# Performance work log

Measured on AMD Instinct MI355X. Metric: run time of the kernel, lower is better.

Reference implementation:

```python
import math
import jax, jax.numpy as jnp
import numpy as np

V = 256; PS = 4; D = 256; MAXR = 4; MINR = 2; WIN = 4; KRET = 8; LAMP = 0.2

def _ln(x, g, b):
    m = x.mean(-1, keepdims=True)
    v = ((x - m) ** 2).mean(-1, keepdims=True)
    return (x - m) / jnp.sqrt(v + 1e-5) * g + b

def _gelu(x):
    return jax.nn.gelu(x, approximate=False)  # torch nn.GELU default = exact erf

def setup_inputs():
    key = jax.random.key(0)
    ks = iter(jax.random.split(key, 64))
    def w(shape, s=0.02):
        return jax.random.normal(next(ks), shape, jnp.float32) * s
    B, T = 32, 2048
    x = jax.random.randint(next(ks), (B, T), 0, V)
    z = lambda *s: jnp.zeros(s, jnp.float32)
    o = lambda *s: jnp.ones(s, jnp.float32)
    return dict(
        x=x,
        emb=w((V, D)), pos=w((PS, D)),
        gru_wih=w((3 * D, D)), gru_whh=w((3 * D, D)), gru_bih=z(3 * D), gru_bhh=z(3 * D),
        pp_ln_g=o(D), pp_ln_b=z(D),
        sum_w=w((D, D)), sum_b=z(D),
        msg_w1=w((2 * D, D)), msg_b1=z(D), msg_w2=w((D, D)), msg_b2=z(D),
        upd_w1=w((2 * D, D)), upd_b1=z(D), upd_w2=w((D, D)), upd_b2=z(D),
        halt_w=w((D, 1)), halt_b=z(1),
        mp_ln_g=o(D), mp_ln_b=z(D),
        q_w=w((D, D)), q_b=z(D), k_w=w((D, D)), k_b=z(D),
        v_w=w((D, D)), v_b=z(D), o_w=w((D, D)), o_b=z(D),
        br_w=w((D, D)), br_b=z(D),
        f_ln_g=o(D), f_ln_b=z(D),
        head_w=w((D, V)),
    )

def _forward(x, emb, pos, gru_wih, gru_whh, gru_bih, gru_bhh, pp_ln_g, pp_ln_b,
             sum_w, sum_b, msg_w1, msg_b1, msg_w2, msg_b2, upd_w1, upd_b1,
             upd_w2, upd_b2, halt_w, halt_b, mp_ln_g, mp_ln_b,
             q_w, q_b, k_w, k_b, v_w, v_b, o_w, o_b, br_w, br_b,
             f_ln_g, f_ln_b, head_w):
    B, T = x.shape
    N = T // PS  # T chosen divisible by patch_size, so F.pad is a no-op
    patches = x.reshape(B * N, PS)
    # --- GRU patch processor (all patches processed identically -> batch them) ---
    hin = emb[patches] + pos[None, :, :]            # [BN, PS, D]
    xg = hin @ gru_wih.T + gru_bih                  # [BN, PS, 3D]
    def gru_step(hprev, xp):
        gh = hprev @ gru_whh.T + gru_bhh
        ir, iz, inn = jnp.split(xp, 3, axis=-1)
        hr, hz, hn = jnp.split(gh, 3, axis=-1)
        r = jax.nn.sigmoid(ir + hr)
        zg = jax.nn.sigmoid(iz + hz)
        n = jnp.tanh(inn + r * hn)
        h = (1 - zg) * n + zg * hprev
        return h, h
    h0 = jnp.zeros((B * N, D), xg.dtype)
    _, seq = jax.lax.scan(gru_step, h0, jnp.swapaxes(xg, 0, 1))
    local = _ln(jnp.swapaxes(seq, 0, 1), pp_ln_g, pp_ln_b).reshape(B, N, PS, D)
    summaries = local.mean(2) @ sum_w + sum_b       # [B, N, D]
    # --- local message passing with ACT halting (vectorized sliding window) ---
    idx = jnp.arange(N)[:, None] + jnp.arange(-WIN, 1)[None, :]
    valid = idx >= 0
    idxc = jnp.clip(idx, 0, N - 1)
    counts = valid.sum(1).astype(jnp.float32)                     # [N]
    h = summaries
    remaining = jnp.ones((B, N, 1), jnp.float32)
    output = jnp.zeros_like(h)
    kl = jnp.float32(0.0)
    for step in range(MAXR):
        nb = h[:, idxc]
        sr = jnp.broadcast_to(h[:, :, None, :], nb.shape)
        m = _gelu(jnp.concatenate([sr, nb], -1) @ msg_w1 + msg_b1) @ msg_w2 + msg_b2
        msgs = (m * valid[None, :, :, None]).sum(2) / counts[None, :, None]
        upd = _gelu(jnp.concatenate([h, msgs], -1) @ upd_w1 + upd_b1) @ upd_w2 + upd_b2
        h = _ln(h + upd, mp_ln_g, mp_ln_b)
        if step < MINR:
            hp = jnp.zeros((B, 1, 1), jnp.float32)
        elif step == MAXR - 1:
            hp = jnp.ones((B, 1, 1), jnp.float32)
        else:
            hp = jax.nn.sigmoid(h.mean(1, keepdims=True) @ halt_w + halt_b)  # [B,1,1]
        output = output + remaining * hp * h
        remaining = remaining * (1 - hp)
        p = LAMP * (1 - LAMP) ** step
        kl = kl + p * (math.log(p) - jnp.log(hp.mean() + 1e-8))
    kl = kl / MAXR
    # --- sparse top-k causal retrieval over patch summaries ---
    q = output @ q_w + q_b
    k = output @ k_w + k_b
    v = output @ v_w + v_b
    scores = jnp.einsum('bnd,bmd->bnm', q, k) / math.sqrt(D)
    causal = jnp.tril(jnp.ones((N, N), bool))
    scores = jnp.where(causal[None], scores, -jnp.inf)
    tv, ti = jax.lax.top_k(scores, KRET)
    bI = jnp.arange(B)[:, None, None]
    nI = jnp.arange(N)[None, :, None]
    sparse = jnp.full_like(scores, -jnp.inf).at[bI, nI, ti].set(tv)
    attn = jax.nn.softmax(sparse, axis=-1)
    retrieved = jnp.einsum('bnm,bmd->bnd', attn, v) @ o_w + o_b
    combined = output + retrieved
    broad = combined @ br_w + br_b                                # [B, N, D]
    final = (local + broad[:, :, None, :]).reshape(B, N * PS, D)
    logits = _ln(final, f_ln_g, f_ln_b) @ head_w                  # [B, T, V]
    return logits, kl

def reference(x, emb, pos, gru_wih, gru_whh, gru_bih, gru_bhh, pp_ln_g, pp_ln_b,
              sum_w, sum_b, msg_w1, msg_b1, msg_w2, msg_b2, upd_w1, upd_b1,
              upd_w2, upd_b2, halt_w, halt_b, mp_ln_g, mp_ln_b,
              q_w, q_b, k_w, k_b, v_w, v_b, o_w, o_b, br_w, br_b,
              f_ln_g, f_ln_b, head_w):
    return _forward(x, emb, pos, gru_wih, gru_whh, gru_bih, gru_bhh, pp_ln_g, pp_ln_b,
                    sum_w, sum_b, msg_w1, msg_b1, msg_w2, msg_b2, upd_w1, upd_b1,
                    upd_w2, upd_b2, halt_w, halt_b, mp_ln_g, mp_ln_b,
                    q_w, q_b, k_w, k_b, v_w, v_b, o_w, o_b, br_w, br_b,
                    f_ln_g, f_ln_b, head_w)
```

## Files before the change

### kernel.cpp

```cpp
#include <hip/hip_runtime.h>
#include <cmath>


constexpr int N_   = 512;
constexpr int B_   = 32;
constexpr int BN_  = B_ * N_;
constexpr int M1_  = BN_ * 4;

typedef short bf16x8 __attribute__((ext_vector_type(8)));
typedef float f32x4  __attribute__((ext_vector_type(4)));

__device__ __forceinline__ float gelu_f(float x) {
  return 0.5f * x * (1.0f + erff(x * 0.70710678118654752440f));
}
__device__ __forceinline__ float sigm_f(float x) {
  return 1.0f / (1.0f + expf(-x));
}
__device__ __forceinline__ unsigned short f2bf(float f) {
  union { float f; unsigned int u; } c; c.f = f;
  unsigned int u = c.u;
  u += 0x7FFFu + ((u >> 16) & 1u);
  return (unsigned short)(u >> 16);
}
__device__ __forceinline__ float bf2f(unsigned short u) {
  union { unsigned int u; float f; } c; c.u = ((unsigned int)u) << 16;
  return c.f;
}
__device__ __forceinline__ int phys(int g, int r) {
  return ((g << 6) | (r ^ g)) << 3;
}
__device__ __forceinline__ int phys128(int g, int r) {
  return ((g << 7) | (r ^ g)) << 3;
}
__device__ __forceinline__ int phys16(int g, int r) {
  return ((g << 4) | (r ^ g)) << 3;
}

template<int AMODE, int EPI, int COUT>
__global__ __launch_bounds__(256)
void gemm_big(const void* __restrict__ A, const unsigned short* __restrict__ Bt,
              const float* __restrict__ bias, void* __restrict__ C,
              int M, int Nn, int K, int bstride, int ldC)
{
  __shared__ short As[4 * 128 * 8];
  __shared__ short Bs[4 * 128 * 8];
  const int t  = threadIdx.x;
  const int m0 = blockIdx.y * 128, n0 = blockIdx.x * 128;
  const int lane = t & 63, w = t >> 6;
  const int wr = w >> 1, wc = w & 1;
  const int fr = lane & 15, fg = lane >> 4;

  f32x4 acc[4][4] = {};

  for (int k0 = 0; k0 < K; k0 += 32) {
    #pragma unroll
    for (int c = 0; c < 2; ++c) {
      int idx = t + c * 256;
      int row = idx >> 2, g = idx & 3;
      int kk = k0 + g * 8;
      bf16x8 av;
      if constexpr (AMODE == 1) {
        av = *(const bf16x8*)&((const unsigned short*)A)[(size_t)(m0 + row) * K + kk];
      } else {
        const float4* p = (const float4*)&((const float*)A)[(size_t)(m0 + row) * K + kk];
        float4 a = p[0], b = p[1];
        av[0]=(short)f2bf(a.x); av[1]=(short)f2bf(a.y); av[2]=(short)f2bf(a.z); av[3]=(short)f2bf(a.w);
        av[4]=(short)f2bf(b.x); av[5]=(short)f2bf(b.y); av[6]=(short)f2bf(b.z); av[7]=(short)f2bf(b.w);
      }
      *(bf16x8*)&As[phys128(g, row)] = av;
      *(bf16x8*)&Bs[phys128(g, row)] =
          *(const bf16x8*)&Bt[(size_t)(n0 + row) * bstride + kk];
    }
    __syncthreads();

    bf16x8 a[4], b[4];
    #pragma unroll
    for (int i = 0; i < 4; ++i)
      a[i] = *(const bf16x8*)&As[phys128(fg, wr * 64 + i * 16 + fr)];
    #pragma unroll
    for (int j = 0; j < 4; ++j)
      b[j] = *(const bf16x8*)&Bs[phys128(fg, wc * 64 + j * 16 + fr)];
    #pragma unroll
    for (int i = 0; i < 4; ++i)
      #pragma unroll
      for (int j = 0; j < 4; ++j)
        acc[i][j] = __builtin_amdgcn_mfma_f32_16x16x32_bf16(a[i], b[j], acc[i][j], 0, 0, 0);
    __syncthreads();
  }

  #pragma unroll
  for (int i = 0; i < 4; ++i)
    #pragma unroll
    for (int j = 0; j < 4; ++j) {
      int col = n0 + wc * 64 + j * 16 + fr;
      float bcol = bias ? bias[col] : 0.0f;
      #pragma unroll
      for (int r = 0; r < 4; ++r) {
        int row = m0 + wr * 64 + i * 16 + fg * 4 + r;
        float vv = acc[i][j][r] + bcol;
        if constexpr (EPI == 1) vv = gelu_f(vv);
        if constexpr (COUT == 0)
          ((float*)C)[(size_t)row * ldC + col] = vv;
        else
          ((unsigned short*)C)[(size_t)row * ldC + col] = f2bf(vv);
      }
    }
}

template<int MODE, int BSRC, int EPI, int COUT>
__global__ __launch_bounds__(256)
void gemm_mfma(const float* __restrict__ A, const void* __restrict__ Bsrc,
               const float* __restrict__ bias, void* __restrict__ C,
               int M, int Nn, int K, int bstride, int ldC,
               const float* __restrict__ P2,
               const float* __restrict__ emb, const float* __restrict__ pos)
{
  __shared__ short As[4 * 64 * 8];
  __shared__ short Bs[4 * 64 * 8];
  const int tid  = threadIdx.x;
  const int m0   = blockIdx.y * 64, n0 = blockIdx.x * 64;
  const int srow = tid >> 2, sg = tid & 3;
  const int lane = tid & 63, w = tid >> 6;
  const int wr   = w >> 1,  wc = w & 1;
  const int fr   = lane & 15, fg = lane >> 4;

  f32x4 acc[2][2] = {};

  for (int k0 = 0; k0 < K; k0 += 32) {
    {
      int m = m0 + srow, k = k0 + sg * 8;
      bf16x8 tv;
      if constexpr (MODE == 10) {
        if (k < 256)
          tv = *(const bf16x8*)&((const unsigned short*)A)[(size_t)m * 256 + k];
        else
          tv = *(const bf16x8*)&((const unsigned short*)P2)[(size_t)m * 256 + (k - 256)];
      } else if constexpr (MODE == 11) {
        if (k < 256) {
          const float4* p = (const float4*)(A + (size_t)m * 256 + k);
          float4 a = p[0], b = p[1];
          tv[0]=(short)f2bf(a.x); tv[1]=(short)f2bf(a.y); tv[2]=(short)f2bf(a.z); tv[3]=(short)f2bf(a.w);
          tv[4]=(short)f2bf(b.x); tv[5]=(short)f2bf(b.y); tv[6]=(short)f2bf(b.z); tv[7]=(short)f2bf(b.w);
        } else {
          tv = *(const bf16x8*)&((const unsigned short*)P2)[(size_t)m * 256 + (k - 256)];
        }
      } else {
        float v[8];
        if constexpr (MODE == 6) {
          const float* src = nullptr;
          if (m < 256) src = emb + (size_t)m * 256 + k;
          else if (m < 260) src = pos + (size_t)(m - 256) * 256 + k;
          if (src) {
            const float4* p = (const float4*)src;
            float4 a = p[0], b = p[1];
            v[0]=a.x; v[1]=a.y; v[2]=a.z; v[3]=a.w; v[4]=b.x; v[5]=b.y; v[6]=b.z; v[7]=b.w;
          } else {
            #pragma unroll
            for (int j = 0; j < 8; ++j) v[j] = 0.f;
          }
        } else if constexpr (MODE == 8) {
          #pragma unroll
          for (int j = 0; j < 8; ++j) v[j] = P2[(size_t)(k + j) * 256 + m];
        } else {
          const unsigned short* Ab = (const unsigned short*)A;
          const unsigned short* base = Ab + (size_t)m * 1024 + k;
          bf16x8 r0 = *(const bf16x8*)(base);
          bf16x8 r1 = *(const bf16x8*)(base + 256);
          bf16x8 r2 = *(const bf16x8*)(base + 512);
          bf16x8 r3 = *(const bf16x8*)(base + 768);
          #pragma unroll
          for (int j = 0; j < 8; ++j)
            v[j] = 0.25f * (bf2f((unsigned short)r0[j]) + bf2f((unsigned short)r1[j]) +
                            bf2f((unsigned short)r2[j]) + bf2f((unsigned short)r3[j]));
        }
        #pragma unroll
        for (int j = 0; j < 8; ++j) tv[j] = (short)f2bf(v[j]);
      }
      *(bf16x8*)&As[phys(sg, srow)] = tv;
    }
    if constexpr (BSRC == 0) {
      const unsigned short* Bt = (const unsigned short*)Bsrc;
      *(bf16x8*)&Bs[phys(sg, srow)] =
          *(const bf16x8*)&Bt[(size_t)(n0 + srow) * bstride + k0 + sg * 8];
    } else {
      const float* Bf = (const float*)Bsrc;
      const float4* p = (const float4*)(Bf + (size_t)(n0 + srow) * bstride + k0 + sg * 8);
      float4 a = p[0], b = p[1];
      bf16x8 tv;
      tv[0]=(short)f2bf(a.x); tv[1]=(short)f2bf(a.y); tv[2]=(short)f2bf(a.z); tv[3]=(short)f2bf(a.w);
      tv[4]=(short)f2bf(b.x); tv[5]=(short)f2bf(b.y); tv[6]=(short)f2bf(b.z); tv[7]=(short)f2bf(b.w);
      *(bf16x8*)&Bs[phys(sg, srow)] = tv;
    }
    __syncthreads();

    bf16x8 a0 = *(const bf16x8*)&As[phys(fg, wr * 32 + fr)];
    bf16x8 a1 = *(const bf16x8*)&As[phys(fg, wr * 32 + 16 + fr)];
    bf16x8 b0 = *(const bf16x8*)&Bs[phys(fg, wc * 32 + fr)];
    bf16x8 b1 = *(const bf16x8*)&Bs[phys(fg, wc * 32 + 16 + fr)];
    acc[0][0] = __builtin_amdgcn_mfma_f32_16x16x32_bf16(a0, b0, acc[0][0], 0, 0, 0);
    acc[0][1] = __builtin_amdgcn_mfma_f32_16x16x32_bf16(a0, b1, acc[0][1], 0, 0, 0);
    acc[1][0] = __builtin_amdgcn_mfma_f32_16x16x32_bf16(a1, b0, acc[1][0], 0, 0, 0);
    acc[1][1] = __builtin_amdgcn_mfma_f32_16x16x32_bf16(a1, b1, acc[1][1], 0, 0, 0);
    __syncthreads();
  }

  #pragma unroll
  for (int i = 0; i < 2; ++i) {
    #pragma unroll
    for (int j = 0; j < 2; ++j) {
      int row0 = m0 + wr * 32 + i * 16 + fg * 4;
      int col  = n0 + wc * 32 + j * 16 + fr;
      float bcol = bias ? bias[col] : 0.0f;
      #pragma unroll
      for (int r = 0; r < 4; ++r) {
        float vv = acc[i][j][r] + bcol;
        if constexpr (EPI == 1) vv = gelu_f(vv);
        int row = row0 + r;
        if constexpr (COUT == 0)
          ((float*)C)[(size_t)row * ldC + col] = vv;
        else
          ((unsigned short*)C)[(size_t)row * ldC + col] = f2bf(vv);
      }
    }
  }
}

template<int OUTM>
__global__ __launch_bounds__(256)
void gemm_ln(const unsigned short* __restrict__ U, const unsigned short* __restrict__ u2T,
             const float* __restrict__ bias, unsigned short* __restrict__ h,
             const float* __restrict__ g, const float* __restrict__ bb,
             const float* __restrict__ hp, float* __restrict__ outp)
{
  __shared__ short As[4 * 16 * 8];
  __shared__ short Bs[4 * 256 * 8];
  __shared__ float psum[4][16], pssq[4][16];
  const int m0 = blockIdx.x * 16;
  const int t  = threadIdx.x;
  const int lane = t & 63, w = t >> 6;
  const int fr = lane & 15, fg = lane >> 4;

  f32x4 acc[4] = {};
  for (int k0 = 0; k0 < 256; k0 += 32) {
    if (t < 64) {
      int row = t >> 2, gq = t & 3;
      *(bf16x8*)&As[phys16(gq, row)] =
          *(const bf16x8*)&U[(size_t)(m0 + row) * 256 + k0 + gq * 8];
    }
    const unsigned short* brow = u2T + (size_t)t * 256 + k0;
    #pragma unroll
    for (int gq = 0; gq < 4; ++gq)
      *(bf16x8*)&Bs[((gq << 8) | (t ^ gq)) << 3] = *(const bf16x8*)(brow + gq * 8);
    __syncthreads();
    bf16x8 a = *(const bf16x8*)&As[phys16(fg, fr)];
    #pragma unroll
    for (int j = 0; j < 4; ++j) {
      int n = 64 * w + 16 * j + fr;
      bf16x8 b = *(const bf16x8*)&Bs[((fg << 8) | (n ^ fg)) << 3];
      acc[j] = __builtin_amdgcn_mfma_f32_16x16x32_bf16(a, b, acc[j], 0, 0, 0);
    }
    __syncthreads();
  }

  float bcol[4], gv[4], bv[4];
  #pragma unroll
  for (int j = 0; j < 4; ++j) {
    int col = 64 * w + 16 * j + fr;
    bcol[j] = bias[col]; gv[j] = g[col]; bv[j] = bb[col];
  }
  float vsum[4] = {}, vssq[4] = {};
  #pragma unroll
  for (int j = 0; j < 4; ++j) {
    int col = 64 * w + 16 * j + fr;
    #pragma unroll
    for (int r = 0; r < 4; ++r) {
      int row = m0 + 4 * fg + r;
      float v = acc[j][r] + bcol[j] + bf2f(h[(size_t)row * 256 + col]);
      acc[j][r] = v;
      vsum[r] += v;
      vssq[r] += v * v;
    }
  }
  #pragma unroll
  for (int off = 1; off < 16; off <<= 1) {
    #pragma unroll
    for (int r = 0; r < 4; ++r) {
      vsum[r] += __shfl_xor(vsum[r], off, 64);
      vssq[r] += __shfl_xor(vssq[r], off, 64);
    }
  }
  if (fr == 0) {
    #pragma unroll
    for (int r = 0; r < 4; ++r) {
      psum[w][4 * fg + r] = vsum[r];
      pssq[w][4 * fg + r] = vssq[r];
    }
  }
  __syncthreads();

  float rem = 0.f;
  if constexpr (OUTM == 3) rem = 1.0f - hp[m0 >> 9];
  #pragma unroll
  for (int r = 0; r < 4; ++r) {
    int rr = 4 * fg + r;
    float s  = psum[0][rr] + psum[1][rr] + psum[2][rr] + psum[3][rr];
    float q2 = pssq[0][rr] + pssq[1][rr] + pssq[2][rr] + pssq[3][rr];
    float mean = s * (1.0f / 256.0f);
    float var  = q2 * (1.0f / 256.0f) - mean * mean;
    float inv  = rsqrtf(var + 1e-5f);
    int row = m0 + rr;
    #pragma unroll
    for (int j = 0; j < 4; ++j) {
      int col = 64 * w + 16 * j + fr;
      float y = (acc[j][r] - mean) * inv * gv[j] + bv[j];
      h[(size_t)row * 256 + col] = f2bf(y);
      if constexpr (OUTM == 3) outp[(size_t)row * 256 + col] += rem * y;
    }
  }
}

__global__ __launch_bounds__(256)
void scores_tri(const unsigned short* __restrict__ qkv, float* __restrict__ sc)
{
  int flat = blockIdx.x;
  int xcd = flat & 7, s = flat >> 3;
  int bhi = s / 36, tile = s - bhi * 36;
  int b = bhi * 8 + xcd;
  int ti = 0;
  while ((ti + 1) * (ti + 2) / 2 <= tile) ++ti;
  int tj = tile - ti * (ti + 1) / 2;
  const int m0 = ti * 64, n0 = tj * 64;
  const unsigned short* Aq = qkv + (size_t)b * N_ * 768;
  const unsigned short* Bk = Aq + 256;

  __shared__ short As[4 * 64 * 8];
  __shared__ short Bs[4 * 64 * 8];
  const int tid  = threadIdx.x;
  const int srow = tid >> 2, sg = tid & 3;
  const int lane = tid & 63, w = tid >> 6;
  const int wr   = w >> 1,  wc = w & 1;
  const int fr   = lane & 15, fg = lane >> 4;

  f32x4 acc[2][2] = {};
  for (int k0 = 0; k0 < 256; k0 += 32) {
    *(bf16x8*)&As[phys(sg, srow)] =
        *(const bf16x8*)&Aq[(size_t)(m0 + srow) * 768 + k0 + sg * 8];
    *(bf16x8*)&Bs[phys(sg, srow)] =
        *(const bf16x8*)&Bk[(size_t)(n0 + srow) * 768 + k0 + sg * 8];
    __syncthreads();
    bf16x8 a0 = *(const bf16x8*)&As[phys(fg, wr * 32 + fr)];
    bf16x8 a1 = *(const bf16x8*)&As[phys(fg, wr * 32 + 16 + fr)];
    bf16x8 b0 = *(const bf16x8*)&Bs[phys(fg, wc * 32 + fr)];
    bf16x8 b1 = *(const bf16x8*)&Bs[phys(fg, wc * 32 + 16 + fr)];
    acc[0][0] = __builtin_amdgcn_mfma_f32_16x16x32_bf16(a0, b0, acc[0][0], 0, 0, 0);
    acc[0][1] = __builtin_amdgcn_mfma_f32_16x16x32_bf16(a0, b1, acc[0][1], 0, 0, 0);
    acc[1][0] = __builtin_amdgcn_mfma_f32_16x16x32_bf16(a1, b0, acc[1][0], 0, 0, 0);
    acc[1][1] = __builtin_amdgcn_mfma_f32_16x16x32_bf16(a1, b1, acc[1][1], 0, 0, 0);
    __syncthreads();
  }
  float* scb = sc + (size_t)b * N_ * N_;
  #pragma unroll
  for (int i = 0; i < 2; ++i) {
    #pragma unroll
    for (int j = 0; j < 2; ++j) {
      int row0 = m0 + wr * 32 + i * 16 + fg * 4;
      int col  = n0 + wc * 32 + j * 16 + fr;
      #pragma unroll
      for (int r = 0; r < 4; ++r) {
        int row = row0 + r;
        float vv = acc[i][j][r] * 0.0625f;
        if (col > row) vv = -__builtin_inff();
        scb[(size_t)row * N_ + col] = vv;
      }
    }
  }
}

struct PrepJobs {
  const float* src[12];
  unsigned short* dst[12];
  int rows[12];
  int dstride[12];
  int strt[12];
};
__global__ __launch_bounds__(256)
void prep_w_k(PrepJobs pj)
{
  int jid = blockIdx.y;
  const float* src = pj.src[jid];
  unsigned short* dst = pj.dst[jid];
  int ds = pj.dstride[jid];
  int total = pj.rows[jid] << 8;
  if (pj.strt[jid]) {
    for (int i = blockIdx.x * 256 + threadIdx.x; i < total; i += gridDim.x * 256) {
      int k = i & 255, n = i >> 8;
      dst[(size_t)n * ds + k] = f2bf(src[i]);
    }
  } else {
    for (int i = blockIdx.x * 256 + threadIdx.x; i < total; i += gridDim.x * 256) {
      int k = i & 255, n = i >> 8;
      dst[(size_t)n * ds + k] = f2bf(src[(size_t)k * 256 + n]);
    }
  }
}

__global__ __launch_bounds__(256)
void biasprep_k(const float* __restrict__ upd_b1, const float* __restrict__ msg_b2,
                const float* __restrict__ upd_w1, const float* __restrict__ msg_b1,
                const float* __restrict__ o_b, const float* __restrict__ br_w,
                const float* __restrict__ br_b, const float* __restrict__ q_b,
                const float* __restrict__ k_b, const float* __restrict__ v_b,
                float* __restrict__ biasU, float* __restrict__ biasHsn,
                float* __restrict__ biasB2, float* __restrict__ bQKV)
{
  int c = threadIdx.x;
  float s = upd_b1[c];
  for (int k = 0; k < 256; ++k)
    s += msg_b2[k] * upd_w1[(size_t)(256 + k) * 256 + c];
  biasU[c] = s;
  biasHsn[c] = msg_b1[c];
  biasHsn[256 + c] = 0.f;
  float s2 = br_b[c];
  for (int k = 0; k < 256; ++k)
    s2 += o_b[k] * br_w[(size_t)k * 256 + c];
  biasB2[c] = s2;
  bQKV[c] = q_b[c]; bQKV[256 + c] = k_b[c]; bQKV[512 + c] = v_b[c];
}

template<int FIRST>
__global__ __launch_bounds__(256)
void gru_pw_k(const unsigned short* __restrict__ gh, const float* __restrict__ bhh,
              const float* __restrict__ embW, const int* __restrict__ x,
              const float* __restrict__ bih,
              unsigned short* __restrict__ h, unsigned short* __restrict__ local, int t)
{
  int i   = blockIdx.x * 256 + threadIdx.x;
  int row = i >> 8, d = i & 255;
  int tok = x[row * 4 + t];
  const float* er = embW + (size_t)tok * 768;
  const float* pr = embW + (size_t)(256 + t) * 768;
  float ir  = er[d]       + pr[d]       + bih[d];
  float iz  = er[256 + d] + pr[256 + d] + bih[256 + d];
  float inn = er[512 + d] + pr[512 + d] + bih[512 + d];
  float hr, hz, hn;
  if constexpr (FIRST) {
    hr = bhh[d]; hz = bhh[256 + d]; hn = bhh[512 + d];
  } else {
    const unsigned short* gr = gh + (size_t)row * 768;
    hr = bf2f(gr[d]); hz = bf2f(gr[256 + d]); hn = bf2f(gr[512 + d]);
  }
  float r  = sigm_f(ir + hr);
  float zg = sigm_f(iz + hz);
  float nn = tanhf(inn + r * hn);
  float hnew;
  if constexpr (FIRST) hnew = (1.0f - zg) * nn;
  else                 hnew = (1.0f - zg) * nn + zg * bf2f(h[i]);
  h[i] = f2bf(hnew);
  local[((size_t)row * 4 + t) * 256 + d] = f2bf(hnew);
}

__global__ __launch_bounds__(256)
void smsg_k(const unsigned short* __restrict__ hsn, unsigned short* __restrict__ S)
{
  int i = blockIdx.x * 256 + threadIdx.x;
  int m = i >> 6, d4 = (i & 63) << 2;
  int n = m & (N_ - 1);
  ushort4 hsu = *(const ushort4*)&hsn[(size_t)m * 512 + d4];
  float hs0 = bf2f(hsu.x), hs1 = bf2f(hsu.y), hs2 = bf2f(hsu.z), hs3 = bf2f(hsu.w);
  float a0 = 0.f, a1 = 0.f, a2 = 0.f, a3 = 0.f;
  #pragma unroll
  for (int kk = 0; kk < 5; ++kk) {
    int idx = n + kk - 4;
    if (idx >= 0) {
      ushort4 hv = *(const ushort4*)&hsn[(size_t)(m + kk - 4) * 512 + 256 + d4];
      a0 += gelu_f(hs0 + bf2f(hv.x));
      a1 += gelu_f(hs1 + bf2f(hv.y));
      a2 += gelu_f(hs2 + bf2f(hv.z));
      a3 += gelu_f(hs3 + bf2f(hv.w));
    }
  }
  float sc1 = 1.0f / (float)((n < 4 ? n : 4) + 1);
  ushort4 o = {f2bf(a0 * sc1), f2bf(a1 * sc1), f2bf(a2 * sc1), f2bf(a3 * sc1)};
  *(ushort4*)&S[(size_t)m * 256 + d4] = o;
}

__global__ __launch_bounds__(256)
void ln_bf16_k(unsigned short* __restrict__ X, const float* __restrict__ g,
               const float* __restrict__ bb)
{
  int wave = threadIdx.x >> 6, lane = threadIdx.x & 63;
  int row  = blockIdx.x * 4 + wave;
  unsigned short* xr = X + (size_t)row * 256;
  ushort4 u = *(const ushort4*)&xr[lane * 4];
  float x[4] = {bf2f(u.x), bf2f(u.y), bf2f(u.z), bf2f(u.w)};
  float s = x[0] + x[1] + x[2] + x[3];
  #pragma unroll
  for (int off = 1; off < 64; off <<= 1) s += __shfl_xor(s, off, 64);
  float mean = s * (1.0f / 256.0f);
  float ss = 0.f;
  #pragma unroll
  for (int j = 0; j < 4; ++j) { float d = x[j] - mean; ss += d * d; }
  #pragma unroll
  for (int off = 1; off < 64; off <<= 1) ss += __shfl_xor(ss, off, 64);
  float inv = rsqrtf(ss * (1.0f / 256.0f) + 1e-5f);
  ushort4 o;
  o.x = f2bf((x[0] - mean) * inv * g[lane*4+0] + bb[lane*4+0]);
  o.y = f2bf((x[1] - mean) * inv * g[lane*4+1] + bb[lane*4+1]);
  o.z = f2bf((x[2] - mean) * inv * g[lane*4+2] + bb[lane*4+2]);
  o.w = f2bf((x[3] - mean) * inv * g[lane*4+3] + bb[lane*4+3]);
  *(ushort4*)&xr[lane * 4] = o;
}

__global__ __launch_bounds__(256)
void ln_cvt_k(const unsigned short* __restrict__ X, const unsigned short* __restrict__ Add,
              const float* __restrict__ g, const float* __restrict__ bb,
              unsigned short* __restrict__ Out)
{
  int wave = threadIdx.x >> 6, lane = threadIdx.x & 63;
  int row  = blockIdx.x * 4 + wave;
  ushort4 u = *(const ushort4*)&X[(size_t)row * 256 + lane * 4];
  ushort4 a = *(const ushort4*)&Add[(size_t)(row >> 2) * 256 + lane * 4];
  float x[4] = {bf2f(u.x) + bf2f(a.x), bf2f(u.y) + bf2f(a.y),
                bf2f(u.z) + bf2f(a.z), bf2f(u.w) + bf2f(a.w)};
  float s = x[0] + x[1] + x[2] + x[3];
  #pragma unroll
  for (int off = 1; off < 64; off <<= 1) s += __shfl_xor(s, off, 64);
  float mean = s * (1.0f / 256.0f);
  float ss = 0.f;
  #pragma unroll
  for (int j = 0; j < 4; ++j) { float d = x[j] - mean; ss += d * d; }
  #pragma unroll
  for (int off = 1; off < 64; off <<= 1) ss += __shfl_xor(ss, off, 64);
  float inv = rsqrtf(ss * (1.0f / 256.0f) + 1e-5f);
  ushort4 o;
  o.x = f2bf((x[0] - mean) * inv * g[lane*4+0] + bb[lane*4+0]);
  o.y = f2bf((x[1] - mean) * inv * g[lane*4+1] + bb[lane*4+1]);
  o.z = f2bf((x[2] - mean) * inv * g[lane*4+2] + bb[lane*4+2]);
  o.w = f2bf((x[3] - mean) * inv * g[lane*4+3] + bb[lane*4+3]);
  *(ushort4*)&Out[(size_t)row * 256 + lane * 4] = o;
}

__global__ __launch_bounds__(256)
void halt1_k(const unsigned short* __restrict__ h, const float* __restrict__ hw,
             float* __restrict__ part)
{
  int b = blockIdx.x, s = blockIdx.y, tid = threadIdx.x;
  const unsigned short* p = h + ((size_t)b * N_ + s * 32) * 256;
  float acc = 0.f;
  for (int i = tid * 4; i < 32 * 256; i += 1024) {
    ushort4 u = *(const ushort4*)&p[i];
    const float4 w4 = *(const float4*)&hw[i & 255];
    acc += bf2f(u.x) * w4.x + bf2f(u.y) * w4.y + bf2f(u.z) * w4.z + bf2f(u.w) * w4.w;
  }
  __shared__ float red[256];
  red[tid] = acc; __syncthreads();
  for (int off = 128; off > 0; off >>= 1) {
    if (tid < off) red[tid] += red[tid + off];
    __syncthreads();
  }
  if (tid == 0) part[b * 16 + s] = red[0];
}
__global__ __launch_bounds__(64)
void halt2_k(const float* __restrict__ part, const float* __restrict__ hb,
             float* __restrict__ hp)
{
  int b = threadIdx.x;
  if (b < 32) {
    float s = 0.f;
    for (int i = 0; i < 16; ++i) s += part[b * 16 + i];
    hp[b] = sigm_f(s * (1.0f / (float)N_) + hb[0]);
  }
}
__global__ __launch_bounds__(256)
void out2_k(const unsigned short* __restrict__ h, const float* __restrict__ hp,
            float* __restrict__ outp)
{
  int i = blockIdx.x * 256 + threadIdx.x;
  outp[i] = hp[i >> 17] * bf2f(h[i]);
}

__global__ __launch_bounds__(256)
void topk_k(const float* __restrict__ sc, const unsigned short* __restrict__ qkv,
            unsigned short* __restrict__ rpre)
{
  const float NEG = -__builtin_inff();
  int wave = threadIdx.x >> 6, lane = threadIdx.x & 63;
  int rowg = blockIdx.x * 4 + wave;
  int b = rowg >> 9, n = rowg & (N_ - 1);
  const float* srow = sc + (size_t)rowg * N_;
  float v[8];
  #pragma unroll
  for (int j = 0; j < 8; ++j) {
    int col = lane + j * 64;
    v[j] = (col <= n) ? srow[col] : NEG;
  }
  float tv[8]; int ti[8];
  #pragma unroll
  for (int it = 0; it < 8; ++it) {
    float bv = v[0]; int bi = lane;
    #pragma unroll
    for (int j = 1; j < 8; ++j)
      if (v[j] > bv) { bv = v[j]; bi = lane + j * 64; }
    #pragma unroll
    for (int off = 1; off < 64; off <<= 1) {
      float ov = __shfl_xor(bv, off, 64);
      int   oi = __shfl_xor(bi, off, 64);
      if (ov > bv || (ov == bv && oi < bi)) { bv = ov; bi = oi; }
    }
    tv[it] = bv; ti[it] = bi;
    if ((bi & 63) == lane) v[bi >> 6] = NEG;
  }
  float mx = tv[0];
  float wsum = 0.f, wj[8];
  #pragma unroll
  for (int j = 0; j < 8; ++j) { wj[j] = expf(tv[j] - mx); wsum += wj[j]; }
  float inv = 1.0f / wsum;
  const unsigned short* vb = qkv + 512;
  int d0 = lane * 4;
  float a0 = 0.f, a1 = 0.f, a2 = 0.f, a3 = 0.f;
  #pragma unroll
  for (int j = 0; j < 8; ++j) {
    float wgt = wj[j] * inv;
    ushort4 vv = *(const ushort4*)&vb[((size_t)(b * N_ + ti[j])) * 768 + d0];
    a0 += wgt * bf2f(vv.x); a1 += wgt * bf2f(vv.y);
    a2 += wgt * bf2f(vv.z); a3 += wgt * bf2f(vv.w);
  }
  ushort4 o = {f2bf(a0), f2bf(a1), f2bf(a2), f2bf(a3)};
  *(ushort4*)&rpre[(size_t)rowg * 256 + d0] = o;
}

__global__ void kl_k(const float* __restrict__ hp, float* __restrict__ out)
{
  if (threadIdx.x == 0 && blockIdx.x == 0) {
    float hm = 0.f;
    for (int b = 0; b < 32; ++b) hm += hp[b];
    hm *= (1.0f / 32.0f);
    const float l1e8 = logf(1e-8f);
    float kl = 0.f;
    kl += 0.2f    * (logf(0.2f)    - l1e8);
    kl += 0.16f   * (logf(0.16f)   - l1e8);
    kl += 0.128f  * (logf(0.128f)  - logf(hm + 1e-8f));
    kl += 0.1024f * (logf(0.1024f) - logf(1.0f + 1e-8f));
    out[0] = kl * 0.25f;
  }
}

extern "C" void kernel_launch(void* const* d_in, const int* in_sizes, int n_in,
                              void* d_out, int out_size, void* d_ws, size_t ws_size,
                              hipStream_t stream)
{
  const int*   x       = (const int*)  d_in[0];
  const float* emb     = (const float*)d_in[1];
  const float* pos     = (const float*)d_in[2];
  const float* gru_wih = (const float*)d_in[3];
  const float* gru_whh = (const float*)d_in[4];
  const float* gru_bih = (const float*)d_in[5];
  const float* gru_bhh = (const float*)d_in[6];
  const float* pp_ln_g = (const float*)d_in[7];
  const float* pp_ln_b = (const float*)d_in[8];
  const float* sum_w   = (const float*)d_in[9];
  const float* sum_b   = (const float*)d_in[10];
  const float* msg_w1  = (const float*)d_in[11];
  const float* msg_b1  = (const float*)d_in[12];
  const float* msg_w2  = (const float*)d_in[13];
  const float* msg_b2  = (const float*)d_in[14];
  const float* upd_w1  = (const float*)d_in[15];
  const float* upd_b1  = (const float*)d_in[16];
  const float* upd_w2  = (const float*)d_in[17];
  const float* upd_b2  = (const float*)d_in[18];
  const float* halt_w  = (const float*)d_in[19];
  const float* halt_b  = (const float*)d_in[20];
  const float* mp_ln_g = (const float*)d_in[21];
  const float* mp_ln_b = (const float*)d_in[22];
  const float* q_w     = (const float*)d_in[23];
  const float* q_b     = (const float*)d_in[24];
  const float* k_w     = (const float*)d_in[25];
  const float* k_b     = (const float*)d_in[26];
  const float* v_w     = (const float*)d_in[27];
  const float* v_b     = (const float*)d_in[28];
  const float* o_w     = (const float*)d_in[29];
  const float* o_b     = (const float*)d_in[30];
  const float* br_w    = (const float*)d_in[31];
  const float* br_b    = (const float*)d_in[32];
  const float* f_ln_g  = (const float*)d_in[33];
  const float* f_ln_b  = (const float*)d_in[34];
  const float* head_w  = (const float*)d_in[35];

  constexpr size_t SZ_Q = (size_t)BN_ * 256;
  float* ws     = (float*)d_ws;
  float* R_h    = ws;
  float* R_outp = R_h    + SZ_Q;
  float* R_b1   = R_outp + SZ_Q;
  float* R_b2   = R_b1   + SZ_Q;
  float* R_b3   = R_b2   + SZ_Q;
  float* R_rp   = R_b3   + SZ_Q;
  unsigned short* R_loc = (unsigned short*)(R_rp + SZ_Q);
  unsigned short* wb = R_loc + 4 * SZ_Q;
  unsigned short* sumT  = wb;
  unsigned short* W1cT  = sumT  + 65536;
  unsigned short* u1cT  = W1cT  + 131072;
  unsigned short* u2T   = u1cT  + 131072;
  unsigned short* qkvT  = u2T   + 65536;
  unsigned short* brWT  = qkvT  + 196608;
  unsigned short* headT = brWT  + 131072;
  unsigned short* whhT  = headT + 65536;
  float* R_embW = (float*)(whhT + 196608);
  float* R_bU   = R_embW + 320 * 768;
  float* R_bH   = R_bU + 256;
  float* R_bB2  = R_bH + 512;
  float* R_bQKV = R_bB2 + 256;
  float* R_part = R_bQKV + 768;
  float* R_hp   = R_part + 512;

  unsigned short* R_hb = ((unsigned short*)R_b3) + SZ_Q;

  float* logits = (float*)d_out;
  dim3 blk(256);

  PrepJobs pj;
  const float* srcs[11] = {sum_w, msg_w1, msg_w1 + 65536, upd_w1, upd_w2,
                           q_w, k_w, v_w, br_w, head_w, gru_whh};
  unsigned short* dsts[11] = {sumT, W1cT, W1cT + 65536, u1cT, u2T,
                              qkvT, qkvT + 65536, qkvT + 131072, brWT, headT, whhT};
  int rows[11] = {256,256,256,256,256,256,256,256,256,256,768};
  int dstd[11] = {256,256,256,512,256,256,256,256,512,256,256};
  int strt[11] = {0,0,0,0,0,0,0,0,0,0,1};
  for (int i = 0; i < 11; ++i) {
    pj.src[i]=srcs[i]; pj.dst[i]=dsts[i]; pj.rows[i]=rows[i];
    pj.dstride[i]=dstd[i]; pj.strt[i]=strt[i];
  }
  prep_w_k<<<dim3(64, 11), blk, 0, stream>>>(pj);
  biasprep_k<<<dim3(1), blk, 0, stream>>>(upd_b1, msg_b2, upd_w1, msg_b1,
                                          o_b, br_w, br_b, q_b, k_b, v_b,
                                          R_bU, R_bH, R_bB2, R_bQKV);
  gemm_mfma<8, 1, 0, 1><<<dim3(4, 4), blk, 0, stream>>>(
      nullptr, msg_w2, nullptr, u1cT + 256, 256, 256, 256, 256, 512,
      upd_w1 + 65536, nullptr, nullptr);
  gemm_mfma<8, 1, 0, 1><<<dim3(4, 4), blk, 0, stream>>>(
      nullptr, o_w, nullptr, brWT + 256, 256, 256, 256, 256, 512,
      br_w, nullptr, nullptr);
  gemm_mfma<6, 1, 0, 0><<<dim3(12, 5), blk, 0, stream>>>(
      nullptr, gru_wih, nullptr, R_embW, 320, 768, 256, 256, 768,
      nullptr, emb, pos);

  unsigned short* ghB = (unsigned short*)R_b1;
  gru_pw_k<1><<<dim3(BN_), blk, 0, stream>>>(
      nullptr, gru_bhh, R_embW, x, gru_bih, R_hb, R_loc, 0);
  for (int t = 1; t < 4; ++t) {
    gemm_big<1, 0, 1><<<dim3(6, 128), blk, 0, stream>>>(
        R_hb, whhT, gru_bhh, ghB, BN_, 768, 256, 256, 768);
    gru_pw_k<0><<<dim3(BN_), blk, 0, stream>>>(
        ghB, gru_bhh, R_embW, x, gru_bih, R_hb, R_loc, t);
  }
  ln_bf16_k<<<dim3(M1_ / 4), blk, 0, stream>>>(R_loc, pp_ln_g, pp_ln_b);

  gemm_mfma<9, 0, 0, 1><<<dim3(4, 256), blk, 0, stream>>>(
      (const float*)R_loc, sumT, sum_b, R_hb, BN_, 256, 256, 256, 256,
      nullptr, nullptr, nullptr);

  unsigned short* hsnB = (unsigned short*)R_b1;
  unsigned short* UB   = (unsigned short*)R_b2;
  unsigned short* Sb   = (unsigned short*)R_b3;
  for (int step = 0; step < 4; ++step) {
    gemm_big<1, 0, 1><<<dim3(4, 128), blk, 0, stream>>>(
        R_hb, W1cT, R_bH, hsnB, BN_, 512, 256, 256, 512);
    smsg_k<<<dim3(BN_ / 4), blk, 0, stream>>>(hsnB, Sb);
    gemm_mfma<10, 0, 1, 1><<<dim3(4, 256), blk, 0, stream>>>(
        (const float*)R_hb, u1cT, R_bU, UB, BN_, 256, 512, 512, 256,
        (const float*)Sb, nullptr, nullptr);
    if (step == 3) {
      gemm_ln<3><<<dim3(BN_ / 16), blk, 0, stream>>>(
          UB, u2T, upd_b2, R_hb, mp_ln_g, mp_ln_b, R_hp, R_outp);
    } else {
      gemm_ln<0><<<dim3(BN_ / 16), blk, 0, stream>>>(
          UB, u2T, upd_b2, R_hb, mp_ln_g, mp_ln_b, nullptr, nullptr);
      if (step == 2) {
        halt1_k<<<dim3(32, 16), blk, 0, stream>>>(R_hb, halt_w, R_part);
        halt2_k<<<dim3(1), dim3(64), 0, stream>>>(R_part, halt_b, R_hp);
        out2_k<<<dim3(BN_), blk, 0, stream>>>(R_hb, R_hp, R_outp);
      }
    }
  }

  unsigned short* qkv  = (unsigned short*)R_b3;
  unsigned short* rpre = ((unsigned short*)R_rp) + SZ_Q;
  float* sc = R_b1;
  gemm_big<0, 0, 1><<<dim3(6, 128), blk, 0, stream>>>(
      R_outp, qkvT, R_bQKV, qkv, BN_, 768, 256, 256, 768);
  scores_tri<<<dim3(1152), blk, 0, stream>>>(qkv, sc);
  topk_k<<<dim3(BN_ / 4), blk, 0, stream>>>(sc, qkv, rpre);

  unsigned short* broadB = (unsigned short*)R_h;
  gemm_mfma<11, 0, 0, 1><<<dim3(4, 256), blk, 0, stream>>>(
      R_outp, brWT, R_bB2, broadB, BN_, 256, 512, 512, 256,
      (const float*)rpre, nullptr, nullptr);

  unsigned short* Abuf = (unsigned short*)R_b1;
  ln_cvt_k<<<dim3(M1_ / 4), blk, 0, stream>>>(R_loc, broadB, f_ln_g, f_ln_b, Abuf);
  gemm_big<1, 0, 0><<<dim3(2, 512), blk, 0, stream>>>(
      Abuf, headT, nullptr, logits, M1_, 256, 256, 256, 256);

  kl_k<<<dim3(1), dim3(64), 0, stream>>>(R_hp, logits + (size_t)M1_ * 256);
}
```

Baseline: 611.8 us.

## Fuse final LayerNorm into head GEMM, store scores in bf16, vectorize pointwise kernels

Adds a head_ln_k kernel that computes the final LayerNorm row statistics in-block and normalizes A tiles while loading them, which removes the separate ln_cvt_k pass and its intermediate buffer. Attention scores are now written and read as bf16 rather than fp32, halving that traffic. gru_pw_k and out2_k are vectorized to process four elements per thread. In exchange, LN inputs are recomputed once per column block, the one-pass variance formula is used, and bf16 scores may change top-k tie ordering.

```diff
diff --git a/kernel.cpp b/kernel.cpp
--- a/kernel.cpp
+++ b/kernel.cpp
@@ -103,6 +103,106 @@
           ((float*)C)[(size_t)row * ldC + col] = vv;
         else
           ((unsigned short*)C)[(size_t)row * ldC + col] = f2bf(vv);
+      }
+    }
+}
+
+__global__ __launch_bounds__(256)
+void head_ln_k(const unsigned short* __restrict__ loc,
+               const unsigned short* __restrict__ broad,
+               const float* __restrict__ g, const float* __restrict__ bb,
+               const unsigned short* __restrict__ headT,
+               float* __restrict__ out)
+{
+  __shared__ short As[4 * 128 * 8];
+  __shared__ short Bs[4 * 128 * 8];
+  __shared__ float sMean[128], sInv[128];
+  const int t  = threadIdx.x;
+  const int m0 = blockIdx.y * 128, n0 = blockIdx.x * 128;
+  const int lane = t & 63, w = t >> 6;
+  const int wr = w >> 1, wc = w & 1;
+  const int fr = lane & 15, fg = lane >> 4;
+
+  {
+    int r = t >> 1, half = t & 1;
+    int row = m0 + r;
+    const unsigned short* lp = loc   + (size_t)row * 256 + half * 128;
+    const unsigned short* bp = broad + (size_t)(row >> 2) * 256 + half * 128;
+    float s = 0.f, ss = 0.f;
+    #pragma unroll
+    for (int c = 0; c < 16; ++c) {
+      bf16x8 u = *(const bf16x8*)(lp + c * 8);
+      bf16x8 a = *(const bf16x8*)(bp + c * 8);
+      #pragma unroll
+      for (int e = 0; e < 8; ++e) {
+        float xv = bf2f((unsigned short)u[e]) + bf2f((unsigned short)a[e]);
+        s += xv; ss += xv * xv;
+      }
+    }
+    s  += __shfl_xor(s, 1, 64);
+    ss += __shfl_xor(ss, 1, 64);
+    if (half == 0) {
+      float mean = s * (1.0f / 256.0f);
+      float var  = ss * (1.0f / 256.0f) - mean * mean;
+      sMean[r] = mean;
+      sInv[r]  = rsqrtf(var + 1e-5f);
+    }
+  }
+  __syncthreads();
+
+  f32x4 acc[4][4] = {};
+  for (int k0 = 0; k0 < 256; k0 += 32) {
+    #pragma unroll
+    for (int c = 0; c < 2; ++c) {
+      int idx = t + c * 256;
+      int row = idx >> 2, gq = idx & 3;
+      int kk = k0 + gq * 8;
+      int grow = m0 + row;
+      bf16x8 u = *(const bf16x8*)&loc[(size_t)grow * 256 + kk];
+      bf16x8 a = *(const bf16x8*)&broad[(size_t)(grow >> 2) * 256 + kk];
+      float mean = sMean[row], inv = sInv[row];
+      const float4 g0 = *(const float4*)(g + kk);
+      const float4 g1 = *(const float4*)(g + kk + 4);
+      const float4 v0 = *(const float4*)(bb + kk);
+      const float4 v1 = *(const float4*)(bb + kk + 4);
+      float gv[8] = {g0.x,g0.y,g0.z,g0.w,g1.x,g1.y,g1.z,g1.w};
+      float bv[8] = {v0.x,v0.y,v0.z,v0.w,v1.x,v1.y,v1.z,v1.w};
+      bf16x8 av;
+      #pragma unroll
+      for (int e = 0; e < 8; ++e) {
+        float xv = bf2f((unsigned short)u[e]) + bf2f((unsigned short)a[e]);
+        av[e] = (short)f2bf((xv - mean) * inv * gv[e] + bv[e]);
+      }
+      *(bf16x8*)&As[phys128(gq, row)] = av;
+      *(bf16x8*)&Bs[phys128(gq, row)] =
+          *(const bf16x8*)&headT[(size_t)(n0 + row) * 256 + kk];
+    }
+    __syncthreads();
+
+    bf16x8 a[4], b[4];
+    #pragma unroll
+    for (int i = 0; i < 4; ++i)
+      a[i] = *(const bf16x8*)&As[phys128(fg, wr * 64 + i * 16 + fr)];
+    #pragma unroll
+    for (int j = 0; j < 4; ++j)
+      b[j] = *(const bf16x8*)&Bs[phys128(fg, wc * 64 + j * 16 + fr)];
+    #pragma unroll
+    for (int i = 0; i < 4; ++i)
+      #pragma unroll
+      for (int j = 0; j < 4; ++j)
+        acc[i][j] = __builtin_amdgcn_mfma_f32_16x16x32_bf16(a[i], b[j], acc[i][j], 0, 0, 0);
+    __syncthreads();
+  }
+
+  #pragma unroll
+  for (int i = 0; i < 4; ++i)
+    #pragma unroll
+    for (int j = 0; j < 4; ++j) {
+      int col = n0 + wc * 64 + j * 16 + fr;
+      #pragma unroll
+      for (int r = 0; r < 4; ++r) {
+        int row = m0 + wr * 64 + i * 16 + fg * 4 + r;
+        out[(size_t)row * 256 + col] = acc[i][j][r];
       }
     }
 }
@@ -320,7 +420,7 @@
 }
 
 __global__ __launch_bounds__(256)
-void scores_tri(const unsigned short* __restrict__ qkv, float* __restrict__ sc)
+void scores_tri(const unsigned short* __restrict__ qkv, unsigned short* __restrict__ sc)
 {
   int flat = blockIdx.x;
   int xcd = flat & 7, s = flat >> 3;
@@ -358,7 +458,7 @@
     acc[1][1] = __builtin_amdgcn_mfma_f32_16x16x32_bf16(a1, b1, acc[1][1], 0, 0, 0);
     __syncthreads();
   }
-  float* scb = sc + (size_t)b * N_ * N_;
+  unsigned short* scb = sc + (size_t)b * N_ * N_;
   #pragma unroll
   for (int i = 0; i < 2; ++i) {
     #pragma unroll
@@ -370,7 +470,7 @@
         int row = row0 + r;
         float vv = acc[i][j][r] * 0.0625f;
         if (col > row) vv = -__builtin_inff();
-        scb[(size_t)row * N_ + col] = vv;
+        scb[(size_t)row * N_ + col] = f2bf(vv);
       }
     }
   }
@@ -435,28 +535,55 @@
               unsigned short* __restrict__ h, unsigned short* __restrict__ local, int t)
 {
   int i   = blockIdx.x * 256 + threadIdx.x;
-  int row = i >> 8, d = i & 255;
+  int row = i >> 6, d0 = (i & 63) << 2;
   int tok = x[row * 4 + t];
   const float* er = embW + (size_t)tok * 768;
   const float* pr = embW + (size_t)(256 + t) * 768;
-  float ir  = er[d]       + pr[d]       + bih[d];
-  float iz  = er[256 + d] + pr[256 + d] + bih[256 + d];
-  float inn = er[512 + d] + pr[512 + d] + bih[512 + d];
-  float hr, hz, hn;
+  float4 e0 = *(const float4*)(er + d0);
+  float4 e1 = *(const float4*)(er + 256 + d0);
+  float4 e2 = *(const float4*)(er + 512 + d0);
+  float4 p0 = *(const float4*)(pr + d0);
+  float4 p1 = *(const float4*)(pr + 256 + d0);
+  float4 p2 = *(const float4*)(pr + 512 + d0);
+  float4 q0 = *(const float4*)(bih + d0);
+  float4 q1 = *(const float4*)(bih + 256 + d0);
+  float4 q2 = *(const float4*)(bih + 512 + d0);
+  float ir[4]  = {e0.x+p0.x+q0.x, e0.y+p0.y+q0.y, e0.z+p0.z+q0.z, e0.w+p0.w+q0.w};
+  float iz[4]  = {e1.x+p1.x+q1.x, e1.y+p1.y+q1.y, e1.z+p1.z+q1.z, e1.w+p1.w+q1.w};
+  float inn[4] = {e2.x+p2.x+q2.x, e2.y+p2.y+q2.y, e2.z+p2.z+q2.z, e2.w+p2.w+q2.w};
+  float hr[4], hz[4], hn[4];
   if constexpr (FIRST) {
-    hr = bhh[d]; hz = bhh[256 + d]; hn = bhh[512 + d];
+    float4 b0 = *(const float4*)(bhh + d0);
+    float4 b1 = *(const float4*)(bhh + 256 + d0);
+    float4 b2 = *(const float4*)(bhh + 512 + d0);
+    hr[0]=b0.x; hr[1]=b0.y; hr[2]=b0.z; hr[3]=b0.w;
+    hz[0]=b1.x; hz[1]=b1.y; hz[2]=b1.z; hz[3]=b1.w;
+    hn[0]=b2.x; hn[1]=b2.y; hn[2]=b2.z; hn[3]=b2.w;
   } else {
     const unsigned short* gr = gh + (size_t)row * 768;
-    hr = bf2f(gr[d]); hz = bf2f(gr[256 + d]); hn = bf2f(gr[512 + d]);
-  }
-  float r  = sigm_f(ir + hr);
-  float zg = sigm_f(iz + hz);
-  float nn = tanhf(inn + r * hn);
-  float hnew;
-  if constexpr (FIRST) hnew = (1.0f - zg) * nn;
-  else                 hnew = (1.0f - zg) * nn + zg * bf2f(h[i]);
-  h[i] = f2bf(hnew);
-  local[((size_t)row * 4 + t) * 256 + d] = f2bf(hnew);
+    ushort4 u0 = *(const ushort4*)(gr + d0);
+    ushort4 u1 = *(const ushort4*)(gr + 256 + d0);
+    ushort4 u2 = *(const ushort4*)(gr + 512 + d0);
+    hr[0]=bf2f(u0.x); hr[1]=bf2f(u0.y); hr[2]=bf2f(u0.z); hr[3]=bf2f(u0.w);
+    hz[0]=bf2f(u1.x); hz[1]=bf2f(u1.y); hz[2]=bf2f(u1.z); hz[3]=bf2f(u1.w);
+    hn[0]=bf2f(u2.x); hn[1]=bf2f(u2.y); hn[2]=bf2f(u2.z); hn[3]=bf2f(u2.w);
+  }
+  ushort4 hprev = {0, 0, 0, 0};
+  if constexpr (!FIRST) hprev = *(const ushort4*)&h[(size_t)row * 256 + d0];
+  float hp4[4] = {bf2f(hprev.x), bf2f(hprev.y), bf2f(hprev.z), bf2f(hprev.w)};
+  ushort4 oh;
+  #pragma unroll
+  for (int e = 0; e < 4; ++e) {
+    float r  = sigm_f(ir[e] + hr[e]);
+    float zg = sigm_f(iz[e] + hz[e]);
+    float nn = tanhf(inn[e] + r * hn[e]);
+    float hnew;
+    if constexpr (FIRST) hnew = (1.0f - zg) * nn;
+    else                 hnew = (1.0f - zg) * nn + zg * hp4[e];
+    ((unsigned short*)&oh)[e] = f2bf(hnew);
+  }
+  *(ushort4*)&h[(size_t)row * 256 + d0] = oh;
+  *(ushort4*)&local[((size_t)row * 4 + t) * 256 + d0] = oh;
 }
 
 __global__ __launch_bounds__(256)
@@ -512,35 +639,6 @@
 }
 
 __global__ __launch_bounds__(256)
-void ln_cvt_k(const unsigned short* __restrict__ X, const unsigned short* __restrict__ Add,
-              const float* __restrict__ g, const float* __restrict__ bb,
-              unsigned short* __restrict__ Out)
-{
-  int wave = threadIdx.x >> 6, lane = threadIdx.x & 63;
-  int row  = blockIdx.x * 4 + wave;
-  ushort4 u = *(const ushort4*)&X[(size_t)row * 256 + lane * 4];
-  ushort4 a = *(const ushort4*)&Add[(size_t)(row >> 2) * 256 + lane * 4];
-  float x[4] = {bf2f(u.x) + bf2f(a.x), bf2f(u.y) + bf2f(a.y),
-                bf2f(u.z) + bf2f(a.z), bf2f(u.w) + bf2f(a.w)};
-  float s = x[0] + x[1] + x[2] + x[3];
-  #pragma unroll
-  for (int off = 1; off < 64; off <<= 1) s += __shfl_xor(s, off, 64);
-  float mean = s * (1.0f / 256.0f);
-  float ss = 0.f;
-  #pragma unroll
-  for (int j = 0; j < 4; ++j) { float d = x[j] - mean; ss += d * d; }
-  #pragma unroll
-  for (int off = 1; off < 64; off <<= 1) ss += __shfl_xor(ss, off, 64);
-  float inv = rsqrtf(ss * (1.0f / 256.0f) + 1e-5f);
-  ushort4 o;
-  o.x = f2bf((x[0] - mean) * inv * g[lane*4+0] + bb[lane*4+0]);
-  o.y = f2bf((x[1] - mean) * inv * g[lane*4+1] + bb[lane*4+1]);
-  o.z = f2bf((x[2] - mean) * inv * g[lane*4+2] + bb[lane*4+2]);
-  o.w = f2bf((x[3] - mean) * inv * g[lane*4+3] + bb[lane*4+3]);
-  *(ushort4*)&Out[(size_t)row * 256 + lane * 4] = o;
-}
-
-__global__ __launch_bounds__(256)
 void halt1_k(const unsigned short* __restrict__ h, const float* __restrict__ hw,
              float* __restrict__ part)
 {
@@ -576,23 +674,26 @@
             float* __restrict__ outp)
 {
   int i = blockIdx.x * 256 + threadIdx.x;
-  outp[i] = hp[i >> 17] * bf2f(h[i]);
-}
-
-__global__ __launch_bounds__(256)
-void topk_k(const float* __restrict__ sc, const unsigned short* __restrict__ qkv,
+  float hpv = hp[i >> 15];
+  ushort4 u = *(const ushort4*)&h[(size_t)i * 4];
+  float4 o = {hpv * bf2f(u.x), hpv * bf2f(u.y), hpv * bf2f(u.z), hpv * bf2f(u.w)};
+  *(float4*)&outp[(size_t)i * 4] = o;
+}
+
+__global__ __launch_bounds__(256)
+void topk_k(const unsigned short* __restrict__ sc, const unsigned short* __restrict__ qkv,
             unsigned short* __restrict__ rpre)
 {
   const float NEG = -__builtin_inff();
   int wave = threadIdx.x >> 6, lane = threadIdx.x & 63;
   int rowg = blockIdx.x * 4 + wave;
   int b = rowg >> 9, n = rowg & (N_ - 1);
-  const float* srow = sc + (size_t)rowg * N_;
+  const unsigned short* srow = sc + (size_t)rowg * N_;
   float v[8];
   #pragma unroll
   for (int j = 0; j < 8; ++j) {
     int col = lane + j * 64;
-    v[j] = (col <= n) ? srow[col] : NEG;
+    v[j] = (col <= n) ? bf2f(srow[col]) : NEG;
   }
   float tv[8]; int ti[8];
   #pragma unroll
@@ -744,12 +845,12 @@
       nullptr, emb, pos);
 
   unsigned short* ghB = (unsigned short*)R_b1;
-  gru_pw_k<1><<<dim3(BN_), blk, 0, stream>>>(
+  gru_pw_k<1><<<dim3(BN_ / 4), blk, 0, stream>>>(
       nullptr, gru_bhh, R_embW, x, gru_bih, R_hb, R_loc, 0);
   for (int t = 1; t < 4; ++t) {
     gemm_big<1, 0, 1><<<dim3(6, 128), blk, 0, stream>>>(
         R_hb, whhT, gru_bhh, ghB, BN_, 768, 256, 256, 768);
-    gru_pw_k<0><<<dim3(BN_), blk, 0, stream>>>(
+    gru_pw_k<0><<<dim3(BN_ / 4), blk, 0, stream>>>(
         ghB, gru_bhh, R_embW, x, gru_bih, R_hb, R_loc, t);
   }
   ln_bf16_k<<<dim3(M1_ / 4), blk, 0, stream>>>(R_loc, pp_ln_g, pp_ln_b);
@@ -777,14 +878,14 @@
       if (step == 2) {
         halt1_k<<<dim3(32, 16), blk, 0, stream>>>(R_hb, halt_w, R_part);
         halt2_k<<<dim3(1), dim3(64), 0, stream>>>(R_part, halt_b, R_hp);
-        out2_k<<<dim3(BN_), blk, 0, stream>>>(R_hb, R_hp, R_outp);
+        out2_k<<<dim3(BN_ / 4), blk, 0, stream>>>(R_hb, R_hp, R_outp);
       }
     }
   }
 
   unsigned short* qkv  = (unsigned short*)R_b3;
   unsigned short* rpre = ((unsigned short*)R_rp) + SZ_Q;
-  float* sc = R_b1;
+  unsigned short* sc   = (unsigned short*)R_b1;
   gemm_big<0, 0, 1><<<dim3(6, 128), blk, 0, stream>>>(
       R_outp, qkvT, R_bQKV, qkv, BN_, 768, 256, 256, 768);
   scores_tri<<<dim3(1152), blk, 0, stream>>>(qkv, sc);
@@ -795,10 +896,8 @@
       R_outp, brWT, R_bB2, broadB, BN_, 256, 512, 512, 256,
       (const float*)rpre, nullptr, nullptr);
 
-  unsigned short* Abuf = (unsigned short*)R_b1;
-  ln_cvt_k<<<dim3(M1_ / 4), blk, 0, stream>>>(R_loc, broadB, f_ln_g, f_ln_b, Abuf);
-  gemm_big<1, 0, 0><<<dim3(2, 512), blk, 0, stream>>>(
-      Abuf, headT, nullptr, logits, M1_, 256, 256, 256, 256);
+  head_ln_k<<<dim3(2, 512), blk, 0, stream>>>(
+      R_loc, broadB, f_ln_g, f_ln_b, headT, logits);
 
   kl_k<<<dim3(1), dim3(64), 0, stream>>>(R_hp, logits + (size_t)M1_ * 256);
 }
```

After: 620.3 us. Within noise of the previous version (+1.4%).
